# Performance work log

Hardware: AMD Instinct MI355X
Metric: run time of the kernel (lower is better)

## Reference

```python
import jax, jax.numpy as jnp
import numpy as np

N_USERS = 100_000
N_ITEMS = 50_000
EMBED_DIM = 64
N_LAYERS = 2
ALPHA = 0.1
NNZ = 1_600_000
AVG_DEG = 16.0


def setup_inputs() -> dict:
    key = jax.random.key(0)
    ks = jax.random.split(key, 8)
    # COO edge lists for A_ui (user<-item) and A_iu (item<-user).
    ui_rows = jax.random.randint(ks[0], (NNZ,), 0, N_USERS, dtype=jnp.int32)
    ui_cols = jax.random.randint(ks[1], (NNZ,), 0, N_ITEMS, dtype=jnp.int32)
    iu_rows = jax.random.randint(ks[2], (NNZ,), 0, N_ITEMS, dtype=jnp.int32)
    iu_cols = jax.random.randint(ks[3], (NNZ,), 0, N_USERS, dtype=jnp.int32)
    # Row-normalized values ~ 1/degree (module builds D^{-1} R).
    ui_vals = jax.random.uniform(ks[4], (NNZ,), dtype=jnp.float32) * (1.0 / AVG_DEG)
    iu_vals = jax.random.uniform(ks[5], (NNZ,), dtype=jnp.float32) * (1.0 / AVG_DEG)
    # Xavier-style init embeddings.
    user_emb0 = jax.random.normal(ks[6], (N_USERS, EMBED_DIM), dtype=jnp.float32) * 0.01
    item_emb0 = jax.random.normal(ks[7], (N_ITEMS, EMBED_DIM), dtype=jnp.float32) * 0.01
    return {
        "user_emb0": user_emb0, "item_emb0": item_emb0,
        "ui_vals": ui_vals, "iu_vals": iu_vals,
        "ui_rows": ui_rows, "ui_cols": ui_cols,
        "iu_rows": iu_rows, "iu_cols": iu_cols,
    }


def _spmm(rows, cols, vals, x, n_rows):
    # y[r] = sum_e vals[e] * x[cols[e]] for edges with rows[e]==r  (COO SpMM)
    return jax.ops.segment_sum(vals[:, None] * x[cols], rows, num_segments=n_rows)


def reference(user_emb0, item_emb0, ui_vals, iu_vals, ui_rows, ui_cols, iu_rows, iu_cols):
    u_layers = [user_emb0]
    i_layers = [item_emb0]
    for _ in range(N_LAYERS):
        u_new = _spmm(ui_rows, ui_cols, ui_vals, i_layers[-1], N_USERS) + ALPHA * user_emb0
        i_new = _spmm(iu_rows, iu_cols, iu_vals, u_layers[-1], N_ITEMS) + ALPHA * item_emb0
        u_layers.append(u_new)
        i_layers.append(i_new)
    # [(n_layers+1), n_users+n_items, d] -- users and items stacked per layer
    return jnp.stack([jnp.concatenate([u, i], axis=0)
                      for u, i in zip(u_layers, i_layers)])
```

## Files before the change

kernel.cpp:

```cpp
#include <hip/hip_runtime.h>

#define NUSERS 100000
#define NITEMS 50000
#define DIM 64
#define NNZ 1600000
#define ALPHA 0.1f
#define TROWS (NUSERS + NITEMS)
#define LSTRIDE (TROWS * DIM)
#define NEDGES (2 * NNZ)

#define NBUCK_U ((NUSERS + 63) / 64)
#define NBUCK_I ((NITEMS + 31) / 32)
#define NBUCK (NBUCK_U + NBUCK_I)
#define NSCAT_U ((NUSERS + 255) / 256)
#define NSCAT_I ((NITEMS + 127) / 128)
#define NSCAT (NSCAT_U + NSCAT_I)
#define SEG_IBASE (NSCAT_U * 64)
#define NSEG_PAD (NSCAT * 64)

#define CH4 512
#define NCHUNK_H ((NNZ / 4 + CH4 - 1) / CH4)
#define CH_S 8192
#define NCHUNK_S ((NEDGES + CH_S - 1) / CH_S)

typedef float vfloat4 __attribute__((ext_vector_type(4)));

__device__ __forceinline__ unsigned short f2bf(float f) {
    unsigned u = __float_as_uint(f);
    unsigned r = (u + 0x7FFFu + ((u >> 16) & 1u)) >> 16;
    return (unsigned short)r;
}

__device__ __forceinline__ float bf_lo(unsigned u) { return __uint_as_float(u << 16); }
__device__ __forceinline__ float bf_hi(unsigned u) { return __uint_as_float(u & 0xFFFF0000u); }

__global__ __launch_bounds__(256) void init_copy_kernel(const float4* __restrict__ ue,
                                                        const float4* __restrict__ ie,
                                                        float4* __restrict__ out,
                                                        ushort4* __restrict__ xb0) {
    const int nU4 = NUSERS * DIM / 4;
    const int nT4 = TROWS * DIM / 4;
    int i = blockIdx.x * 256 + threadIdx.x;
    if (i >= nT4) return;
    float4 v = (i < nU4) ? ue[i] : ie[i - nU4];
    out[i] = v;
    ushort4 b;
    b.x = f2bf(v.x); b.y = f2bf(v.y); b.z = f2bf(v.z); b.w = f2bf(v.w);
    xb0[i] = b;
}

__global__ __launch_bounds__(256) void bucket_hist_kernel(const int4* __restrict__ ui_rows4,
                                                          const int4* __restrict__ iu_rows4,
                                                          int* __restrict__ gcounts) {
    __shared__ int h[NSCAT];
    for (int t = threadIdx.x; t < NSCAT; t += 256) h[t] = 0;
    __syncthreads();
    int base = blockIdx.x * CH4;
    const int n4 = NNZ / 4;
    for (int j = threadIdx.x; j < CH4; j += 256) {
        int i = base + j;
        if (i >= n4) break;
        int4 ru = ui_rows4[i];
        atomicAdd(&h[ru.x >> 8], 1);
        atomicAdd(&h[ru.y >> 8], 1);
        atomicAdd(&h[ru.z >> 8], 1);
        atomicAdd(&h[ru.w >> 8], 1);
        int4 ri = iu_rows4[i];
        atomicAdd(&h[NSCAT_U + (ri.x >> 7)], 1);
        atomicAdd(&h[NSCAT_U + (ri.y >> 7)], 1);
        atomicAdd(&h[NSCAT_U + (ri.z >> 7)], 1);
        atomicAdd(&h[NSCAT_U + (ri.w >> 7)], 1);
    }
    __syncthreads();
    for (int t = threadIdx.x; t < NSCAT; t += 256) {
        int c = h[t];
        if (c) atomicAdd(&gcounts[t], c);
    }
}

__global__ void scan_buckets_kernel(const int* __restrict__ gcounts,
                                    int* __restrict__ gbase,
                                    int* __restrict__ gcursor) {
    int lane = threadIdx.x;
    int carry = 0;
    for (int b0 = 0; b0 < NSCAT; b0 += 64) {
        int idx = b0 + lane;
        int c = (idx < NSCAT) ? gcounts[idx] : 0;
        int x = c;
        for (int off = 1; off < 64; off <<= 1) {
            int u = __shfl_up(x, off, 64);
            if (lane >= off) x += u;
        }
        int excl = carry + x - c;
        if (idx < NSCAT) { gbase[idx] = excl; gcursor[idx] = excl; }
        carry += __shfl(x, 63, 64);
    }
}

__global__ __launch_bounds__(512) void bin_scatter_kernel(
    const int* __restrict__ ui_rows, const int* __restrict__ ui_cols,
    const float* __restrict__ ui_vals,
    const int* __restrict__ iu_rows, const int* __restrict__ iu_cols,
    const float* __restrict__ iu_vals,
    int* __restrict__ gcursor, int2* __restrict__ binned)
{
    __shared__ int h[NSCAT];
    __shared__ int bbase[NSCAT];
    for (int t = threadIdx.x; t < NSCAT; t += 512) h[t] = 0;
    __syncthreads();
    int base = blockIdx.x * CH_S;
    for (int j = threadIdx.x; j < CH_S; j += 512) {
        int i = base + j;
        if (i >= NEDGES) break;
        int bkt;
        if (i < NNZ) bkt = ui_rows[i] >> 8;
        else         bkt = NSCAT_U + (iu_rows[i - NNZ] >> 7);
        atomicAdd(&h[bkt], 1);
    }
    __syncthreads();
    for (int t = threadIdx.x; t < NSCAT; t += 512) {
        int c = h[t];
        bbase[t] = c ? atomicAdd(&gcursor[t], c) : 0;
        h[t] = 0;
    }
    __syncthreads();
    for (int j = threadIdx.x; j < CH_S; j += 512) {
        int i = base + j;
        if (i >= NEDGES) break;
        int bkt, rl, src; float val;
        if (i < NNZ) {
            int r = ui_rows[i];
            bkt = r >> 8; rl = r & 255;
            src = NUSERS + ui_cols[i]; val = ui_vals[i];
        } else {
            int k = i - NNZ;
            int r = iu_rows[k];
            bkt = NSCAT_U + (r >> 7); rl = r & 127;
            src = iu_cols[k]; val = iu_vals[k];
        }
        int off = atomicAdd(&h[bkt], 1);
        binned[bbase[bkt] + off] = make_int2(src | (rl << 18), __float_as_int(val));
    }
}

__global__ __launch_bounds__(512) void csr_bin_sort_kernel(
    const int* __restrict__ gbase, const int* __restrict__ gcounts,
    const int2* __restrict__ binned, int2* __restrict__ binned2,
    int2* __restrict__ segptr)
{
    __shared__ int h[1024];
    __shared__ int off[1024];
    __shared__ int cur[1024];
    __shared__ int s2[512];
    int cb = blockIdx.x;
    bool isu = (cb < NSCAT_U);
    int s = gbase[cb];
    int n = gcounts[cb];
    int t = threadIdx.x;
    h[t] = 0; h[t + 512] = 0;
    __syncthreads();
    for (int k = t; k < n; k += 512) {
        unsigned w = (unsigned)binned[s + k].x;
        int rl = (int)(w >> 18);
        int src = (int)(w & 0x3FFFFu);
        int bs = isu ? (rl >> 2) : (rl >> 1);
        atomicAdd(&h[bs * 16 + (src >> 14)], 1);
    }
    __syncthreads();
    int e0 = h[2 * t], e1 = h[2 * t + 1];
    int ps = e0 + e1;
    s2[t] = ps;
    __syncthreads();
    for (int d = 1; d < 512; d <<= 1) {
        int v = (t >= d) ? s2[t - d] : 0;
        __syncthreads();
        s2[t] += v;
        __syncthreads();
    }
    int exclp = s2[t] - ps;
    off[2 * t] = exclp + e0;
    off[2 * t + 1] = exclp + e0 + e1;
    cur[2 * t] = exclp;
    cur[2 * t + 1] = exclp + e0;
    __syncthreads();
    if (t < 64) {
        int start = s + ((t == 0) ? 0 : off[t * 16 - 1]);
        int end   = s + off[t * 16 + 15];
        int gseg = isu ? (cb * 64 + t)
                       : (SEG_IBASE + (cb - NSCAT_U) * 64 + t);
        segptr[gseg] = make_int2(start, end);
    }
    for (int k = t; k < n; k += 512) {
        int2 m = binned[s + k];
        unsigned w = (unsigned)m.x;
        int rl = (int)(w >> 18);
        int src = (int)(w & 0x3FFFFu);
        int bs = isu ? (rl >> 2) : (rl >> 1);
        int sub = isu ? (rl & 3) : (rl & 1);
        int pos = atomicAdd(&cur[bs * 16 + (src >> 14)], 1);
        binned2[s + pos] = make_int2(src | (sub << 18), m.y);
    }
}

#define EDGE_ACC4(m, xw)                                                      \
    do {                                                                      \
        unsigned rr = ((unsigned)(m).x >> 18) & 3u;                           \
        float v = __int_as_float((m).y);                                      \
        float xv0 = bf_lo((xw).x), xv1 = bf_hi((xw).x);                       \
        float xv2 = bf_lo((xw).y), xv3 = bf_hi((xw).y);                       \
        float p0 = (rr == 0u) ? v : 0.f;                                      \
        float p1 = (rr == 1u) ? v : 0.f;                                      \
        float p2 = (rr == 2u) ? v : 0.f;                                      \
        float p3 = (rr == 3u) ? v : 0.f;                                      \
        a0.x = fmaf(p0, xv0, a0.x); a0.y = fmaf(p0, xv1, a0.y);               \
        a0.z = fmaf(p0, xv2, a0.z); a0.w = fmaf(p0, xv3, a0.w);               \
        a1.x = fmaf(p1, xv0, a1.x); a1.y = fmaf(p1, xv1, a1.y);               \
        a1.z = fmaf(p1, xv2, a1.z); a1.w = fmaf(p1, xv3, a1.w);               \
        a2.x = fmaf(p2, xv0, a2.x); a2.y = fmaf(p2, xv1, a2.y);               \
        a2.z = fmaf(p2, xv2, a2.z); a2.w = fmaf(p2, xv3, a2.w);               \
        a3.x = fmaf(p3, xv0, a3.x); a3.y = fmaf(p3, xv1, a3.y);               \
        a3.z = fmaf(p3, xv2, a3.z); a3.w = fmaf(p3, xv3, a3.w);               \
    } while (0)

#define EDGE_ACC2(m, xw)                                                      \
    do {                                                                      \
        unsigned rr = ((unsigned)(m).x >> 18) & 1u;                           \
        float v = __int_as_float((m).y);                                      \
        float xv0 = bf_lo((xw).x), xv1 = bf_hi((xw).x);                       \
        float xv2 = bf_lo((xw).y), xv3 = bf_hi((xw).y);                       \
        float p0 = rr ? 0.f : v;                                              \
        float p1 = rr ? v : 0.f;                                              \
        a0.x = fmaf(p0, xv0, a0.x); a0.y = fmaf(p0, xv1, a0.y);               \
        a0.z = fmaf(p0, xv2, a0.z); a0.w = fmaf(p0, xv3, a0.w);               \
        a1.x = fmaf(p1, xv0, a1.x); a1.y = fmaf(p1, xv1, a1.y);               \
        a1.z = fmaf(p1, xv2, a1.z); a1.w = fmaf(p1, xv3, a1.w);               \
    } while (0)

#define ROW_OUT(ar, r, BOUND)                                                 \
    do {                                                                      \
        int row = row0 + (r);                                                 \
        if (row < (BOUND)) {                                                  \
            size_t obase = (size_t)row * DIM + l16 * 4;                       \
            uint2 eb = *(const uint2*)(xb0 + obase);                          \
            vfloat4 o;                                                        \
            o.x = fmaf(ALPHA, bf_lo(eb.x), (ar).x);                           \
            o.y = fmaf(ALPHA, bf_hi(eb.x), (ar).y);                           \
            o.z = fmaf(ALPHA, bf_lo(eb.y), (ar).z);                           \
            o.w = fmaf(ALPHA, bf_hi(eb.y), (ar).w);                           \
            __builtin_nontemporal_store(o, (vfloat4*)(outL + obase));         \
            if (WRITE_BF16) {                                                 \
                ushort4 bb;                                                   \
                bb.x = f2bf(o.x); bb.y = f2bf(o.y);                           \
                bb.z = f2bf(o.z); bb.w = f2bf(o.w);                           \
                *(ushort4*)(xb_next + obase) = bb;                            \
            }                                                                 \
        }                                                                     \
    } while (0)

template <int WRITE_BF16>
__global__ __launch_bounds__(256) void pull_seg_kernel(
    const int2* __restrict__ segptr,
    const int2* __restrict__ cc,
    const unsigned short* __restrict__ xb_prev,
    const unsigned short* __restrict__ xb0,
    float* __restrict__ outL,
    unsigned short* __restrict__ xb_next)
{
    int b = blockIdx.x;
    int wid = threadIdx.x >> 6;
    int lane = threadIdx.x & 63;
    int grp = lane >> 4;
    int l16 = lane & 15;
    int seg = wid * 4 + grp;

    const unsigned short* xp = xb_prev + l16 * 4;

    if (b < NBUCK_U) {
        int2 sp = segptr[b * 16 + seg];
        int e = sp.x, end = sp.y;
        float4 a0 = make_float4(0.f, 0.f, 0.f, 0.f);
        float4 a1 = a0, a2 = a0, a3 = a0;
        for (; e + 2 <= end; e += 2) {
            int2 m0 = cc[e];
            int2 m1 = cc[e + 1];
            uint2 x0 = *(const uint2*)(xp + (size_t)(m0.x & 0x3FFFF) * DIM);
            uint2 x1 = *(const uint2*)(xp + (size_t)(m1.x & 0x3FFFF) * DIM);
            EDGE_ACC4(m0, x0);
            EDGE_ACC4(m1, x1);
        }
        if (e < end) {
            int2 m0 = cc[e];
            uint2 x0 = *(const uint2*)(xp + (size_t)(m0.x & 0x3FFFF) * DIM);
            EDGE_ACC4(m0, x0);
        }
        int row0 = b * 64 + seg * 4;
        ROW_OUT(a0, 0, NUSERS);
        ROW_OUT(a1, 1, NUSERS);
        ROW_OUT(a2, 2, NUSERS);
        ROW_OUT(a3, 3, NUSERS);
    } else {
        int2 sp = segptr[SEG_IBASE + (b - NBUCK_U) * 16 + seg];
        int e = sp.x, end = sp.y;
        float4 a0 = make_float4(0.f, 0.f, 0.f, 0.f);
        float4 a1 = a0;
        for (; e + 2 <= end; e += 2) {
            int2 m0 = cc[e];
            int2 m1 = cc[e + 1];
            uint2 x0 = *(const uint2*)(xp + (size_t)(m0.x & 0x3FFFF) * DIM);
            uint2 x1 = *(const uint2*)(xp + (size_t)(m1.x & 0x3FFFF) * DIM);
            EDGE_ACC2(m0, x0);
            EDGE_ACC2(m1, x1);
        }
        if (e < end) {
            int2 m0 = cc[e];
            uint2 x0 = *(const uint2*)(xp + (size_t)(m0.x & 0x3FFFF) * DIM);
            EDGE_ACC2(m0, x0);
        }
        int row0 = NUSERS + (b - NBUCK_U) * 32 + seg * 2;
        ROW_OUT(a0, 0, TROWS);
        ROW_OUT(a1, 1, TROWS);
    }
}

__global__ __launch_bounds__(256) void init_out_kernel(const float4* __restrict__ ue,
                                                       const float4* __restrict__ ie,
                                                       float4* __restrict__ out) {
    const int nU4 = NUSERS * DIM / 4;
    const int nT4 = TROWS * DIM / 4;
    int i = blockIdx.x * 256 + threadIdx.x;
    if (i >= nT4) return;
    float4 v = (i < nU4) ? ue[i] : ie[i - nU4];
    out[i] = v;
    float4 a = make_float4(ALPHA * v.x, ALPHA * v.y, ALPHA * v.z, ALPHA * v.w);
    out[nT4 + i] = a;
    out[2 * nT4 + i] = a;
}

__global__ __launch_bounds__(256) void spmm_layer_kernel(
    const int* __restrict__ ui_rows, const int* __restrict__ ui_cols,
    const float* __restrict__ ui_vals,
    const int* __restrict__ iu_rows, const int* __restrict__ iu_cols,
    const float* __restrict__ iu_vals,
    const float* __restrict__ x_items, const float* __restrict__ x_users,
    float* __restrict__ y_users, float* __restrict__ y_items)
{
    unsigned tid = blockIdx.x * 256u + threadIdx.x;
    unsigned d = tid & 63u;
    unsigned e = tid >> 6;
    if (e < NNZ) {
        int r = ui_rows[e];
        int c = ui_cols[e];
        float v = ui_vals[e];
        atomicAdd(&y_users[r * DIM + d], v * x_items[c * DIM + d]);
    } else {
        e -= NNZ;
        if (e < NNZ) {
            int r = iu_rows[e];
            int c = iu_cols[e];
            float v = iu_vals[e];
            atomicAdd(&y_items[r * DIM + d], v * x_users[c * DIM + d]);
        }
    }
}

extern "C" void kernel_launch(void* const* d_in, const int* in_sizes, int n_in,
                              void* d_out, int out_size, void* d_ws, size_t ws_size,
                              hipStream_t stream) {
    const float* ue      = (const float*)d_in[0];
    const float* ie      = (const float*)d_in[1];
    const float* ui_vals = (const float*)d_in[2];
    const float* iu_vals = (const float*)d_in[3];
    const int*   ui_rows = (const int*)d_in[4];
    const int*   ui_cols = (const int*)d_in[5];
    const int*   iu_rows = (const int*)d_in[6];
    const int*   iu_cols = (const int*)d_in[7];
    float* out = (float*)d_out;

    float* L1 = out + (size_t)LSTRIDE;
    float* L2 = out + (size_t)2 * LSTRIDE;

    const size_t NB_PAD = 1024;
    const size_t cnt_bytes    = NB_PAD * 3 * 4;
    const size_t seg_bytes    = (size_t)NSEG_PAD * 8;
    const size_t hdr_bytes    = cnt_bytes + seg_bytes;
    const size_t binned_bytes = (size_t)NEDGES * 8;
    const size_t xb_bytes     = (size_t)TROWS * DIM * 2;
    const size_t need_bf16 = hdr_bytes + 2 * binned_bytes + 2 * xb_bytes;

    if (ws_size < need_bf16) {
        const int nT4 = TROWS * DIM / 4;
        init_out_kernel<<<(nT4 + 255) / 256, 256, 0, stream>>>(
            (const float4*)ue, (const float4*)ie, (float4*)out);
        float* u1 = L1; float* i1 = L1 + (size_t)NUSERS * DIM;
        float* u2 = L2; float* i2 = L2 + (size_t)NUSERS * DIM;
        const unsigned nblocks = (2u * NNZ * 64u) / 256u;
        spmm_layer_kernel<<<nblocks, 256, 0, stream>>>(
            ui_rows, ui_cols, ui_vals, iu_rows, iu_cols, iu_vals, ie, ue, u1, i1);
        spmm_layer_kernel<<<nblocks, 256, 0, stream>>>(
            ui_rows, ui_cols, ui_vals, iu_rows, iu_cols, iu_vals, i1, u1, u2, i2);
        return;
    }

    int* gcounts = (int*)d_ws;
    int* gbase   = gcounts + NB_PAD;
    int* gcursor = gbase + NB_PAD;
    int2* segptr  = (int2*)((char*)d_ws + cnt_bytes);
    int2* binned  = (int2*)((char*)d_ws + hdr_bytes);
    int2* binned2 = (int2*)((char*)binned + binned_bytes);
    unsigned short* xb0 = (unsigned short*)((char*)binned2 + binned_bytes);
    unsigned short* xb1 = xb0 + (size_t)TROWS * DIM;

    hipMemsetAsync(gcounts, 0, NB_PAD * sizeof(int), stream);

    const int nT4 = TROWS * DIM / 4;
    init_copy_kernel<<<(nT4 + 255) / 256, 256, 0, stream>>>(
        (const float4*)ue, (const float4*)ie, (float4*)out, (ushort4*)xb0);

    bucket_hist_kernel<<<NCHUNK_H, 256, 0, stream>>>(
        (const int4*)ui_rows, (const int4*)iu_rows, gcounts);
    scan_buckets_kernel<<<1, 64, 0, stream>>>(gcounts, gbase, gcursor);
    bin_scatter_kernel<<<NCHUNK_S, 512, 0, stream>>>(
        ui_rows, ui_cols, ui_vals, iu_rows, iu_cols, iu_vals, gcursor, binned);
    csr_bin_sort_kernel<<<NSCAT, 512, 0, stream>>>(
        gbase, gcounts, binned, binned2, segptr);

    pull_seg_kernel<1><<<NBUCK, 256, 0, stream>>>(
        segptr, binned2, xb0, xb0, L1, xb1);
    pull_seg_kernel<0><<<NBUCK, 256, 0, stream>>>(
        segptr, binned2, xb1, xb0, L2, nullptr);
}
```

Before: 245.8 us.

## Double scatter bucket width and vectorize accumulation with packed float2 FMAs

Scatter buckets now cover 512 user rows and 256 item rows instead of 256 and 128. That halves the bucket count, which shrinks the shared-memory histograms and the global atomic cursor traffic in the binning kernels. The per-bucket CSR sort kernel moves to 1024 threads with larger shared arrays and emits 128 segments per bucket. Separately, the SpMM accumulators become float2 vectors updated with elementwise FMA, so the compiler can emit packed FMA instructions. Larger buckets mean fewer but bigger sort blocks, and 1024-thread blocks with more shared memory may lower occupancy.

```diff
diff --git a/kernel.cpp b/kernel.cpp
--- a/kernel.cpp
+++ b/kernel.cpp
@@ -12,11 +12,11 @@
 #define NBUCK_U ((NUSERS + 63) / 64)
 #define NBUCK_I ((NITEMS + 31) / 32)
 #define NBUCK (NBUCK_U + NBUCK_I)
-#define NSCAT_U ((NUSERS + 255) / 256)
-#define NSCAT_I ((NITEMS + 127) / 128)
+#define NSCAT_U ((NUSERS + 511) / 512)
+#define NSCAT_I ((NITEMS + 255) / 256)
 #define NSCAT (NSCAT_U + NSCAT_I)
-#define SEG_IBASE (NSCAT_U * 64)
-#define NSEG_PAD (NSCAT * 64)
+#define SEG_IBASE (NSCAT_U * 128)
+#define NSEG_PAD (NSCAT * 128)
 
 #define CH4 512
 #define NCHUNK_H ((NNZ / 4 + CH4 - 1) / CH4)
@@ -24,6 +24,7 @@
 #define NCHUNK_S ((NEDGES + CH_S - 1) / CH_S)
 
 typedef float vfloat4 __attribute__((ext_vector_type(4)));
+typedef float vfloat2 __attribute__((ext_vector_type(2)));
 
 __device__ __forceinline__ unsigned short f2bf(float f) {
     unsigned u = __float_as_uint(f);
@@ -61,15 +62,15 @@
         int i = base + j;
         if (i >= n4) break;
         int4 ru = ui_rows4[i];
-        atomicAdd(&h[ru.x >> 8], 1);
-        atomicAdd(&h[ru.y >> 8], 1);
-        atomicAdd(&h[ru.z >> 8], 1);
-        atomicAdd(&h[ru.w >> 8], 1);
+        atomicAdd(&h[ru.x >> 9], 1);
+        atomicAdd(&h[ru.y >> 9], 1);
+        atomicAdd(&h[ru.z >> 9], 1);
+        atomicAdd(&h[ru.w >> 9], 1);
         int4 ri = iu_rows4[i];
-        atomicAdd(&h[NSCAT_U + (ri.x >> 7)], 1);
-        atomicAdd(&h[NSCAT_U + (ri.y >> 7)], 1);
-        atomicAdd(&h[NSCAT_U + (ri.z >> 7)], 1);
-        atomicAdd(&h[NSCAT_U + (ri.w >> 7)], 1);
+        atomicAdd(&h[NSCAT_U + (ri.x >> 8)], 1);
+        atomicAdd(&h[NSCAT_U + (ri.y >> 8)], 1);
+        atomicAdd(&h[NSCAT_U + (ri.z >> 8)], 1);
+        atomicAdd(&h[NSCAT_U + (ri.w >> 8)], 1);
     }
     __syncthreads();
     for (int t = threadIdx.x; t < NSCAT; t += 256) {
@@ -113,8 +114,8 @@
         int i = base + j;
         if (i >= NEDGES) break;
         int bkt;
-        if (i < NNZ) bkt = ui_rows[i] >> 8;
-        else         bkt = NSCAT_U + (iu_rows[i - NNZ] >> 7);
+        if (i < NNZ) bkt = ui_rows[i] >> 9;
+        else         bkt = NSCAT_U + (iu_rows[i - NNZ] >> 8);
         atomicAdd(&h[bkt], 1);
     }
     __syncthreads();
@@ -130,12 +131,12 @@
         int bkt, rl, src; float val;
         if (i < NNZ) {
             int r = ui_rows[i];
-            bkt = r >> 8; rl = r & 255;
+            bkt = r >> 9; rl = r & 511;
             src = NUSERS + ui_cols[i]; val = ui_vals[i];
         } else {
             int k = i - NNZ;
             int r = iu_rows[k];
-            bkt = NSCAT_U + (r >> 7); rl = r & 127;
+            bkt = NSCAT_U + (r >> 8); rl = r & 255;
             src = iu_cols[k]; val = iu_vals[k];
         }
         int off = atomicAdd(&h[bkt], 1);
@@ -143,23 +144,23 @@
     }
 }
 
-__global__ __launch_bounds__(512) void csr_bin_sort_kernel(
+__global__ __launch_bounds__(1024) void csr_bin_sort_kernel(
     const int* __restrict__ gbase, const int* __restrict__ gcounts,
     const int2* __restrict__ binned, int2* __restrict__ binned2,
     int2* __restrict__ segptr)
 {
-    __shared__ int h[1024];
-    __shared__ int off[1024];
-    __shared__ int cur[1024];
-    __shared__ int s2[512];
+    __shared__ int h[2048];
+    __shared__ int off[2048];
+    __shared__ int cur[2048];
+    __shared__ int s2[1024];
     int cb = blockIdx.x;
     bool isu = (cb < NSCAT_U);
     int s = gbase[cb];
     int n = gcounts[cb];
     int t = threadIdx.x;
-    h[t] = 0; h[t + 512] = 0;
-    __syncthreads();
-    for (int k = t; k < n; k += 512) {
+    h[t] = 0; h[t + 1024] = 0;
+    __syncthreads();
+    for (int k = t; k < n; k += 1024) {
         unsigned w = (unsigned)binned[s + k].x;
         int rl = (int)(w >> 18);
         int src = (int)(w & 0x3FFFFu);
@@ -171,7 +172,7 @@
     int ps = e0 + e1;
     s2[t] = ps;
     __syncthreads();
-    for (int d = 1; d < 512; d <<= 1) {
+    for (int d = 1; d < 1024; d <<= 1) {
         int v = (t >= d) ? s2[t - d] : 0;
         __syncthreads();
         s2[t] += v;
@@ -183,14 +184,14 @@
     cur[2 * t] = exclp;
     cur[2 * t + 1] = exclp + e0;
     __syncthreads();
-    if (t < 64) {
+    if (t < 128) {
         int start = s + ((t == 0) ? 0 : off[t * 16 - 1]);
         int end   = s + off[t * 16 + 15];
-        int gseg = isu ? (cb * 64 + t)
-                       : (SEG_IBASE + (cb - NSCAT_U) * 64 + t);
+        int gseg = isu ? (cb * 128 + t)
+                       : (SEG_IBASE + (cb - NSCAT_U) * 128 + t);
         segptr[gseg] = make_int2(start, end);
     }
-    for (int k = t; k < n; k += 512) {
+    for (int k = t; k < n; k += 1024) {
         int2 m = binned[s + k];
         unsigned w = (unsigned)m.x;
         int rl = (int)(w >> 18);
@@ -206,47 +207,53 @@
     do {                                                                      \
         unsigned rr = ((unsigned)(m).x >> 18) & 3u;                           \
         float v = __int_as_float((m).y);                                      \
-        float xv0 = bf_lo((xw).x), xv1 = bf_hi((xw).x);                       \
-        float xv2 = bf_lo((xw).y), xv3 = bf_hi((xw).y);                       \
+        vfloat2 xlo; xlo.x = bf_lo((xw).x); xlo.y = bf_hi((xw).x);            \
+        vfloat2 xhi; xhi.x = bf_lo((xw).y); xhi.y = bf_hi((xw).y);            \
         float p0 = (rr == 0u) ? v : 0.f;                                      \
         float p1 = (rr == 1u) ? v : 0.f;                                      \
         float p2 = (rr == 2u) ? v : 0.f;                                      \
         float p3 = (rr == 3u) ? v : 0.f;                                      \
-        a0.x = fmaf(p0, xv0, a0.x); a0.y = fmaf(p0, xv1, a0.y);               \
-        a0.z = fmaf(p0, xv2, a0.z); a0.w = fmaf(p0, xv3, a0.w);               \
-        a1.x = fmaf(p1, xv0, a1.x); a1.y = fmaf(p1, xv1, a1.y);               \
-        a1.z = fmaf(p1, xv2, a1.z); a1.w = fmaf(p1, xv3, a1.w);               \
-        a2.x = fmaf(p2, xv0, a2.x); a2.y = fmaf(p2, xv1, a2.y);               \
-        a2.z = fmaf(p2, xv2, a2.z); a2.w = fmaf(p2, xv3, a2.w);               \
-        a3.x = fmaf(p3, xv0, a3.x); a3.y = fmaf(p3, xv1, a3.y);               \
-        a3.z = fmaf(p3, xv2, a3.z); a3.w = fmaf(p3, xv3, a3.w);               \
+        vfloat2 P0; P0.x = p0; P0.y = p0;                                     \
+        vfloat2 P1; P1.x = p1; P1.y = p1;                                     \
+        vfloat2 P2; P2.x = p2; P2.y = p2;                                     \
+        vfloat2 P3; P3.x = p3; P3.y = p3;                                     \
+        a0l = __builtin_elementwise_fma(P0, xlo, a0l);                        \
+        a0h = __builtin_elementwise_fma(P0, xhi, a0h);                        \
+        a1l = __builtin_elementwise_fma(P1, xlo, a1l);                        \
+        a1h = __builtin_elementwise_fma(P1, xhi, a1h);                        \
+        a2l = __builtin_elementwise_fma(P2, xlo, a2l);                        \
+        a2h = __builtin_elementwise_fma(P2, xhi, a2h);                        \
+        a3l = __builtin_elementwise_fma(P3, xlo, a3l);                        \
+        a3h = __builtin_elementwise_fma(P3, xhi, a3h);                        \
     } while (0)
 
 #define EDGE_ACC2(m, xw)                                                      \
     do {                                                                      \
         unsigned rr = ((unsigned)(m).x >> 18) & 1u;                           \
         float v = __int_as_float((m).y);                                      \
-        float xv0 = bf_lo((xw).x), xv1 = bf_hi((xw).x);                       \
-        float xv2 = bf_lo((xw).y), xv3 = bf_hi((xw).y);                       \
+        vfloat2 xlo; xlo.x = bf_lo((xw).x); xlo.y = bf_hi((xw).x);            \
+        vfloat2 xhi; xhi.x = bf_lo((xw).y); xhi.y = bf_hi((xw).y);            \
         float p0 = rr ? 0.f : v;                                              \
         float p1 = rr ? v : 0.f;                                              \
-        a0.x = fmaf(p0, xv0, a0.x); a0.y = fmaf(p0, xv1, a0.y);               \
-        a0.z = fmaf(p0, xv2, a0.z); a0.w = fmaf(p0, xv3, a0.w);               \
-        a1.x = fmaf(p1, xv0, a1.x); a1.y = fmaf(p1, xv1, a1.y);               \
-        a1.z = fmaf(p1, xv2, a1.z); a1.w = fmaf(p1, xv3, a1.w);               \
+        vfloat2 P0; P0.x = p0; P0.y = p0;                                     \
+        vfloat2 P1; P1.x = p1; P1.y = p1;                                     \
+        a0l = __builtin_elementwise_fma(P0, xlo, a0l);                        \
+        a0h = __builtin_elementwise_fma(P0, xhi, a0h);                        \
+        a1l = __builtin_elementwise_fma(P1, xlo, a1l);                        \
+        a1h = __builtin_elementwise_fma(P1, xhi, a1h);                        \
     } while (0)
 
-#define ROW_OUT(ar, r, BOUND)                                                 \
+#define ROW_OUT2(al, ah, r, BOUND)                                            \
     do {                                                                      \
         int row = row0 + (r);                                                 \
         if (row < (BOUND)) {                                                  \
             size_t obase = (size_t)row * DIM + l16 * 4;                       \
             uint2 eb = *(const uint2*)(xb0 + obase);                          \
             vfloat4 o;                                                        \
-            o.x = fmaf(ALPHA, bf_lo(eb.x), (ar).x);                           \
-            o.y = fmaf(ALPHA, bf_hi(eb.x), (ar).y);                           \
-            o.z = fmaf(ALPHA, bf_lo(eb.y), (ar).z);                           \
-            o.w = fmaf(ALPHA, bf_hi(eb.y), (ar).w);                           \
+            o.x = fmaf(ALPHA, bf_lo(eb.x), (al).x);                           \
+            o.y = fmaf(ALPHA, bf_hi(eb.x), (al).y);                           \
+            o.z = fmaf(ALPHA, bf_lo(eb.y), (ah).x);                           \
+            o.w = fmaf(ALPHA, bf_hi(eb.y), (ah).y);                           \
             __builtin_nontemporal_store(o, (vfloat4*)(outL + obase));         \
             if (WRITE_BF16) {                                                 \
                 ushort4 bb;                                                   \
@@ -274,12 +281,13 @@
     int seg = wid * 4 + grp;
 
     const unsigned short* xp = xb_prev + l16 * 4;
+    vfloat2 z; z.x = 0.f; z.y = 0.f;
 
     if (b < NBUCK_U) {
         int2 sp = segptr[b * 16 + seg];
         int e = sp.x, end = sp.y;
-        float4 a0 = make_float4(0.f, 0.f, 0.f, 0.f);
-        float4 a1 = a0, a2 = a0, a3 = a0;
+        vfloat2 a0l = z, a0h = z, a1l = z, a1h = z;
+        vfloat2 a2l = z, a2h = z, a3l = z, a3h = z;
         for (; e + 2 <= end; e += 2) {
             int2 m0 = cc[e];
             int2 m1 = cc[e + 1];
@@ -294,15 +302,14 @@
             EDGE_ACC4(m0, x0);
         }
         int row0 = b * 64 + seg * 4;
-        ROW_OUT(a0, 0, NUSERS);
-        ROW_OUT(a1, 1, NUSERS);
-        ROW_OUT(a2, 2, NUSERS);
-        ROW_OUT(a3, 3, NUSERS);
+        ROW_OUT2(a0l, a0h, 0, NUSERS);
+        ROW_OUT2(a1l, a1h, 1, NUSERS);
+        ROW_OUT2(a2l, a2h, 2, NUSERS);
+        ROW_OUT2(a3l, a3h, 3, NUSERS);
     } else {
         int2 sp = segptr[SEG_IBASE + (b - NBUCK_U) * 16 + seg];
         int e = sp.x, end = sp.y;
-        float4 a0 = make_float4(0.f, 0.f, 0.f, 0.f);
-        float4 a1 = a0;
+        vfloat2 a0l = z, a0h = z, a1l = z, a1h = z;
         for (; e + 2 <= end; e += 2) {
             int2 m0 = cc[e];
             int2 m1 = cc[e + 1];
@@ -317,8 +324,8 @@
             EDGE_ACC2(m0, x0);
         }
         int row0 = NUSERS + (b - NBUCK_U) * 32 + seg * 2;
-        ROW_OUT(a0, 0, TROWS);
-        ROW_OUT(a1, 1, TROWS);
+        ROW_OUT2(a0l, a0h, 0, TROWS);
+        ROW_OUT2(a1l, a1h, 1, TROWS);
     }
 }
 
@@ -379,7 +386,7 @@
     float* L1 = out + (size_t)LSTRIDE;
     float* L2 = out + (size_t)2 * LSTRIDE;
 
-    const size_t NB_PAD = 1024;
+    const size_t NB_PAD = 512;
     const size_t cnt_bytes    = NB_PAD * 3 * 4;
     const size_t seg_bytes    = (size_t)NSEG_PAD * 8;
     const size_t hdr_bytes    = cnt_bytes + seg_bytes;
@@ -421,7 +428,7 @@
     scan_buckets_kernel<<<1, 64, 0, stream>>>(gcounts, gbase, gcursor);
     bin_scatter_kernel<<<NCHUNK_S, 512, 0, stream>>>(
         ui_rows, ui_cols, ui_vals, iu_rows, iu_cols, iu_vals, gcursor, binned);
-    csr_bin_sort_kernel<<<NSCAT, 512, 0, stream>>>(
+    csr_bin_sort_kernel<<<NSCAT, 1024, 0, stream>>>(
         gbase, gcounts, binned, binned2, segptr);
 
     pull_seg_kernel<1><<<NBUCK, 256, 0, stream>>>(
```

Result: no change. 243.2 us (-1.0%).

## Widen scatter buckets to 512/256 rows and shuffle-broadcast edge metadata in pull kernel

Applied to the files above, without the earlier changes.

The coarse scatter buckets double in size (512 user rows, 256 item rows), which halves the bucket count. The CSR sort kernel grows to 1024 threads with larger shared histograms to match, and the segment pointer layout changes to 128 segments per bucket. The pull kernel now has each 16-lane group load 8 edge records cooperatively and broadcast them with shuffles, replacing per-lane redundant loads of the same edge. The cost is fewer, larger sort blocks with a longer scan, plus extra shuffle instructions in the inner loop.

```diff
diff --git a/kernel.cpp b/kernel.cpp
--- a/kernel.cpp
+++ b/kernel.cpp
@@ -12,11 +12,11 @@
 #define NBUCK_U ((NUSERS + 63) / 64)
 #define NBUCK_I ((NITEMS + 31) / 32)
 #define NBUCK (NBUCK_U + NBUCK_I)
-#define NSCAT_U ((NUSERS + 255) / 256)
-#define NSCAT_I ((NITEMS + 127) / 128)
+#define NSCAT_U ((NUSERS + 511) / 512)
+#define NSCAT_I ((NITEMS + 255) / 256)
 #define NSCAT (NSCAT_U + NSCAT_I)
-#define SEG_IBASE (NSCAT_U * 64)
-#define NSEG_PAD (NSCAT * 64)
+#define SEG_IBASE (NSCAT_U * 128)
+#define NSEG_PAD (NSCAT * 128)
 
 #define CH4 512
 #define NCHUNK_H ((NNZ / 4 + CH4 - 1) / CH4)
@@ -61,15 +61,15 @@
         int i = base + j;
         if (i >= n4) break;
         int4 ru = ui_rows4[i];
-        atomicAdd(&h[ru.x >> 8], 1);
-        atomicAdd(&h[ru.y >> 8], 1);
-        atomicAdd(&h[ru.z >> 8], 1);
-        atomicAdd(&h[ru.w >> 8], 1);
+        atomicAdd(&h[ru.x >> 9], 1);
+        atomicAdd(&h[ru.y >> 9], 1);
+        atomicAdd(&h[ru.z >> 9], 1);
+        atomicAdd(&h[ru.w >> 9], 1);
         int4 ri = iu_rows4[i];
-        atomicAdd(&h[NSCAT_U + (ri.x >> 7)], 1);
-        atomicAdd(&h[NSCAT_U + (ri.y >> 7)], 1);
-        atomicAdd(&h[NSCAT_U + (ri.z >> 7)], 1);
-        atomicAdd(&h[NSCAT_U + (ri.w >> 7)], 1);
+        atomicAdd(&h[NSCAT_U + (ri.x >> 8)], 1);
+        atomicAdd(&h[NSCAT_U + (ri.y >> 8)], 1);
+        atomicAdd(&h[NSCAT_U + (ri.z >> 8)], 1);
+        atomicAdd(&h[NSCAT_U + (ri.w >> 8)], 1);
     }
     __syncthreads();
     for (int t = threadIdx.x; t < NSCAT; t += 256) {
@@ -113,8 +113,8 @@
         int i = base + j;
         if (i >= NEDGES) break;
         int bkt;
-        if (i < NNZ) bkt = ui_rows[i] >> 8;
-        else         bkt = NSCAT_U + (iu_rows[i - NNZ] >> 7);
+        if (i < NNZ) bkt = ui_rows[i] >> 9;
+        else         bkt = NSCAT_U + (iu_rows[i - NNZ] >> 8);
         atomicAdd(&h[bkt], 1);
     }
     __syncthreads();
@@ -130,12 +130,12 @@
         int bkt, rl, src; float val;
         if (i < NNZ) {
             int r = ui_rows[i];
-            bkt = r >> 8; rl = r & 255;
+            bkt = r >> 9; rl = r & 511;
             src = NUSERS + ui_cols[i]; val = ui_vals[i];
         } else {
             int k = i - NNZ;
             int r = iu_rows[k];
-            bkt = NSCAT_U + (r >> 7); rl = r & 127;
+            bkt = NSCAT_U + (r >> 8); rl = r & 255;
             src = iu_cols[k]; val = iu_vals[k];
         }
         int off = atomicAdd(&h[bkt], 1);
@@ -143,23 +143,23 @@
     }
 }
 
-__global__ __launch_bounds__(512) void csr_bin_sort_kernel(
+__global__ __launch_bounds__(1024) void csr_bin_sort_kernel(
     const int* __restrict__ gbase, const int* __restrict__ gcounts,
     const int2* __restrict__ binned, int2* __restrict__ binned2,
     int2* __restrict__ segptr)
 {
-    __shared__ int h[1024];
-    __shared__ int off[1024];
-    __shared__ int cur[1024];
-    __shared__ int s2[512];
+    __shared__ int h[2048];
+    __shared__ int off[2048];
+    __shared__ int cur[2048];
+    __shared__ int s2[1024];
     int cb = blockIdx.x;
     bool isu = (cb < NSCAT_U);
     int s = gbase[cb];
     int n = gcounts[cb];
     int t = threadIdx.x;
-    h[t] = 0; h[t + 512] = 0;
-    __syncthreads();
-    for (int k = t; k < n; k += 512) {
+    h[t] = 0; h[t + 1024] = 0;
+    __syncthreads();
+    for (int k = t; k < n; k += 1024) {
         unsigned w = (unsigned)binned[s + k].x;
         int rl = (int)(w >> 18);
         int src = (int)(w & 0x3FFFFu);
@@ -171,7 +171,7 @@
     int ps = e0 + e1;
     s2[t] = ps;
     __syncthreads();
-    for (int d = 1; d < 512; d <<= 1) {
+    for (int d = 1; d < 1024; d <<= 1) {
         int v = (t >= d) ? s2[t - d] : 0;
         __syncthreads();
         s2[t] += v;
@@ -183,14 +183,14 @@
     cur[2 * t] = exclp;
     cur[2 * t + 1] = exclp + e0;
     __syncthreads();
-    if (t < 64) {
+    if (t < 128) {
         int start = s + ((t == 0) ? 0 : off[t * 16 - 1]);
         int end   = s + off[t * 16 + 15];
-        int gseg = isu ? (cb * 64 + t)
-                       : (SEG_IBASE + (cb - NSCAT_U) * 64 + t);
+        int gseg = isu ? (cb * 128 + t)
+                       : (SEG_IBASE + (cb - NSCAT_U) * 128 + t);
         segptr[gseg] = make_int2(start, end);
     }
-    for (int k = t; k < n; k += 512) {
+    for (int k = t; k < n; k += 1024) {
         int2 m = binned[s + k];
         unsigned w = (unsigned)m.x;
         int rl = (int)(w >> 18);
@@ -202,12 +202,13 @@
     }
 }
 
-#define EDGE_ACC4(m, xw)                                                      \
+#define EDGE_ACC4(mx, my)                                                     \
     do {                                                                      \
-        unsigned rr = ((unsigned)(m).x >> 18) & 3u;                           \
-        float v = __int_as_float((m).y);                                      \
-        float xv0 = bf_lo((xw).x), xv1 = bf_hi((xw).x);                       \
-        float xv2 = bf_lo((xw).y), xv3 = bf_hi((xw).y);                       \
+        unsigned rr = ((unsigned)(mx) >> 18) & 3u;                            \
+        float v = __int_as_float(my);                                         \
+        uint2 xw = *(const uint2*)(xp + (size_t)((mx) & 0x3FFFF) * DIM);      \
+        float xv0 = bf_lo(xw.x), xv1 = bf_hi(xw.x);                           \
+        float xv2 = bf_lo(xw.y), xv3 = bf_hi(xw.y);                           \
         float p0 = (rr == 0u) ? v : 0.f;                                      \
         float p1 = (rr == 1u) ? v : 0.f;                                      \
         float p2 = (rr == 2u) ? v : 0.f;                                      \
@@ -222,12 +223,13 @@
         a3.z = fmaf(p3, xv2, a3.z); a3.w = fmaf(p3, xv3, a3.w);               \
     } while (0)
 
-#define EDGE_ACC2(m, xw)                                                      \
+#define EDGE_ACC2(mx, my)                                                     \
     do {                                                                      \
-        unsigned rr = ((unsigned)(m).x >> 18) & 1u;                           \
-        float v = __int_as_float((m).y);                                      \
-        float xv0 = bf_lo((xw).x), xv1 = bf_hi((xw).x);                       \
-        float xv2 = bf_lo((xw).y), xv3 = bf_hi((xw).y);                       \
+        unsigned rr = ((unsigned)(mx) >> 18) & 1u;                            \
+        float v = __int_as_float(my);                                         \
+        uint2 xw = *(const uint2*)(xp + (size_t)((mx) & 0x3FFFF) * DIM);      \
+        float xv0 = bf_lo(xw.x), xv1 = bf_hi(xw.x);                           \
+        float xv2 = bf_lo(xw.y), xv3 = bf_hi(xw.y);                           \
         float p0 = rr ? 0.f : v;                                              \
         float p1 = rr ? v : 0.f;                                              \
         a0.x = fmaf(p0, xv0, a0.x); a0.y = fmaf(p0, xv1, a0.y);               \
@@ -271,6 +273,7 @@
     int lane = threadIdx.x & 63;
     int grp = lane >> 4;
     int l16 = lane & 15;
+    int gb = lane & 48;
     int seg = wid * 4 + grp;
 
     const unsigned short* xp = xb_prev + l16 * 4;
@@ -280,18 +283,19 @@
         int e = sp.x, end = sp.y;
         float4 a0 = make_float4(0.f, 0.f, 0.f, 0.f);
         float4 a1 = a0, a2 = a0, a3 = a0;
-        for (; e + 2 <= end; e += 2) {
+        while (e + 8 <= end) {
+            int2 my = cc[e + (l16 & 7)];
+#pragma unroll
+            for (int j = 0; j < 8; ++j) {
+                int mx = __shfl(my.x, gb + j, 64);
+                int mv = __shfl(my.y, gb + j, 64);
+                EDGE_ACC4(mx, mv);
+            }
+            e += 8;
+        }
+        for (; e < end; ++e) {
             int2 m0 = cc[e];
-            int2 m1 = cc[e + 1];
-            uint2 x0 = *(const uint2*)(xp + (size_t)(m0.x & 0x3FFFF) * DIM);
-            uint2 x1 = *(const uint2*)(xp + (size_t)(m1.x & 0x3FFFF) * DIM);
-            EDGE_ACC4(m0, x0);
-            EDGE_ACC4(m1, x1);
-        }
-        if (e < end) {
-            int2 m0 = cc[e];
-            uint2 x0 = *(const uint2*)(xp + (size_t)(m0.x & 0x3FFFF) * DIM);
-            EDGE_ACC4(m0, x0);
+            EDGE_ACC4(m0.x, m0.y);
         }
         int row0 = b * 64 + seg * 4;
         ROW_OUT(a0, 0, NUSERS);
@@ -303,18 +307,19 @@
         int e = sp.x, end = sp.y;
         float4 a0 = make_float4(0.f, 0.f, 0.f, 0.f);
         float4 a1 = a0;
-        for (; e + 2 <= end; e += 2) {
+        while (e + 8 <= end) {
+            int2 my = cc[e + (l16 & 7)];
+#pragma unroll
+            for (int j = 0; j < 8; ++j) {
+                int mx = __shfl(my.x, gb + j, 64);
+                int mv = __shfl(my.y, gb + j, 64);
+                EDGE_ACC2(mx, mv);
+            }
+            e += 8;
+        }
+        for (; e < end; ++e) {
             int2 m0 = cc[e];
-            int2 m1 = cc[e + 1];
-            uint2 x0 = *(const uint2*)(xp + (size_t)(m0.x & 0x3FFFF) * DIM);
-            uint2 x1 = *(const uint2*)(xp + (size_t)(m1.x & 0x3FFFF) * DIM);
-            EDGE_ACC2(m0, x0);
-            EDGE_ACC2(m1, x1);
-        }
-        if (e < end) {
-            int2 m0 = cc[e];
-            uint2 x0 = *(const uint2*)(xp + (size_t)(m0.x & 0x3FFFF) * DIM);
-            EDGE_ACC2(m0, x0);
+            EDGE_ACC2(m0.x, m0.y);
         }
         int row0 = NUSERS + (b - NBUCK_U) * 32 + seg * 2;
         ROW_OUT(a0, 0, TROWS);
@@ -379,7 +384,7 @@
     float* L1 = out + (size_t)LSTRIDE;
     float* L2 = out + (size_t)2 * LSTRIDE;
 
-    const size_t NB_PAD = 1024;
+    const size_t NB_PAD = 512;
     const size_t cnt_bytes    = NB_PAD * 3 * 4;
     const size_t seg_bytes    = (size_t)NSEG_PAD * 8;
     const size_t hdr_bytes    = cnt_bytes + seg_bytes;
@@ -421,7 +426,7 @@
     scan_buckets_kernel<<<1, 64, 0, stream>>>(gcounts, gbase, gcursor);
     bin_scatter_kernel<<<NCHUNK_S, 512, 0, stream>>>(
         ui_rows, ui_cols, ui_vals, iu_rows, iu_cols, iu_vals, gcursor, binned);
-    csr_bin_sort_kernel<<<NSCAT, 512, 0, stream>>>(
+    csr_bin_sort_kernel<<<NSCAT, 1024, 0, stream>>>(
         gbase, gcounts, binned, binned2, segptr);
 
     pull_seg_kernel<1><<<NBUCK, 256, 0, stream>>>(
```

Result: faster. 232.2 us (-5.5%).
